# Kernel tuning notes

Hardware: AMD Instinct MI355X
Metric: run time of the kernel (lower is better)

The kernel has to match this reference:

```python
import jax, jax.numpy as jnp
import numpy as np

B = 2048       # batch
F_IN = 1024    # input feature dim
R_EMB = 1024   # rows of EmbedLinear sparse weight (new features)
NNZ_E = 65536  # nnz of embed sparse weight
F_OUT = 1024   # output dim of ExpandingLinear
NNZ_W = 131072 # nnz of main sparse weight [F_OUT, F_IN + R_EMB]
NNZ_B = 512    # nnz of sparse bias
F_MID = F_IN + R_EMB


def setup_inputs() -> dict:
    key = jax.random.key(0)
    ks = jax.random.split(key, 9)
    return {
        "x": jax.random.normal(ks[0], (B, F_IN), jnp.float32),
        "embed_rows": jax.random.randint(ks[1], (NNZ_E,), 0, R_EMB, jnp.int32),
        "embed_cols": jax.random.randint(ks[2], (NNZ_E,), 0, F_IN, jnp.int32),
        "embed_vals": jax.random.normal(ks[3], (NNZ_E,), jnp.float32) * 0.05,
        "w_rows": jax.random.randint(ks[4], (NNZ_W,), 0, F_OUT, jnp.int32),
        "w_cols": jax.random.randint(ks[5], (NNZ_W,), 0, F_MID, jnp.int32),
        "w_vals": jax.random.normal(ks[6], (NNZ_W,), jnp.float32) * 0.05,
        "bias_idx": jax.random.randint(ks[7], (NNZ_B,), 0, F_OUT, jnp.int32),
        "bias_vals": jax.random.normal(ks[8], (NNZ_B,), jnp.float32),
    }


def _spmm(rows, cols, vals, x, n_rows):
    # sparse COO [n_rows, F] @ x.T -> transposed: returns [B, n_rows]
    # (matches torch.sparse.mm(sparse_w, input.t()).t())
    g = vals[:, None] * x.T[cols]                              # [nnz, B] gather + scale
    return jax.ops.segment_sum(g, rows, num_segments=n_rows).T # scatter-add over rows


def reference(x, embed_rows, embed_cols, embed_vals,
              w_rows, w_cols, w_vals, bias_idx, bias_vals):
    # EmbedLinear.forward: sparse mm + ReLU + concat along features
    h = jax.nn.relu(_spmm(embed_rows, embed_cols, embed_vals, x, R_EMB))  # [B, R_EMB]
    x2 = jnp.concatenate([x, h], axis=1)                                   # [B, F_MID]
    # ExpandingLinear tail: sparse weight mm + densified sparse bias
    bias = jnp.zeros((F_OUT,), x.dtype).at[bias_idx].add(bias_vals)
    return _spmm(w_rows, w_cols, w_vals, x2, F_OUT) + bias[None, :]        # [B, F_OUT]
```

## Files before the change

kernel.cpp:

```cpp
#include <hip/hip_runtime.h>
#include <hip/hip_bf16.h>

#define B_SZ   2048
#define F_IN   1024
#define R_EMB  1024
#define F_OUT  1024
#define F_MID  2048
#define NNZ_E  65536
#define NNZ_W  131072
#define NNZ_B  512

typedef __bf16 bf16x8 __attribute__((ext_vector_type(8)));
typedef float  f32x4  __attribute__((ext_vector_type(4)));

__device__ inline void gload16(const void* g, void* l) {
    __builtin_amdgcn_global_load_lds(
        (const __attribute__((address_space(1))) void*)g,
        (__attribute__((address_space(3))) void*)l, 16, 0, 0);
}

__device__ inline ushort f2bf(float v) {
    __hip_bfloat16 h = __float2bfloat16(v);
    return *reinterpret_cast<ushort*>(&h);
}

__global__ void k_zero4(float4* __restrict__ p, int n) {
    int i = blockIdx.x * blockDim.x + threadIdx.x;
    if (i < n) p[i] = make_float4(0.f, 0.f, 0.f, 0.f);
}

__global__ void k_scatter_fused(const int* __restrict__ er, const int* __restrict__ ec,
                                const float* __restrict__ ev,
                                const int* __restrict__ wr_, const int* __restrict__ wc_,
                                const float* __restrict__ wv,
                                const int* __restrict__ bi, const float* __restrict__ bv,
                                float* __restrict__ Ef, float* __restrict__ Wf,
                                float* __restrict__ biasd) {
    int b = blockIdx.x, t = threadIdx.x;
    if (b < NNZ_E / 256) {
        int i = b * 256 + t;
        atomicAdd(&Ef[(size_t)er[i] * F_IN + ec[i]], ev[i]);
    } else if (b < NNZ_E / 256 + NNZ_W / 256) {
        int i = (b - NNZ_E / 256) * 256 + t;
        atomicAdd(&Wf[(size_t)wr_[i] * F_MID + wc_[i]], wv[i]);
    } else {
        int i = t;
        atomicAdd(&biasd[bi[i]], bv[i]);
        i += 256;
        atomicAdd(&biasd[bi[i]], bv[i]);
    }
}

__global__ void k_cvt_fused(const float4* __restrict__ x, ushort* __restrict__ x2,
                            const float4* __restrict__ Ef, ushort* __restrict__ Ebf,
                            const float4* __restrict__ Wf, ushort* __restrict__ Wbf) {
    int b = blockIdx.x, t = threadIdx.x;
    if (b < 2048) {
        int i = b * 256 + t;
        int row = i >> 8, c4 = i & 255;
        float4 v = x[i];
        ((ushort4*)x2)[(size_t)row * (F_MID / 4) + c4] =
            make_ushort4(f2bf(v.x), f2bf(v.y), f2bf(v.z), f2bf(v.w));
    } else if (b < 3072) {
        int i = (b - 2048) * 256 + t;
        float4 v = Ef[i];
        ((ushort4*)Ebf)[i] = make_ushort4(f2bf(v.x), f2bf(v.y), f2bf(v.z), f2bf(v.w));
    } else {
        int i = (b - 3072) * 256 + t;
        float4 v = Wf[i];
        ((ushort4*)Wbf)[i] = make_ushort4(f2bf(v.x), f2bf(v.y), f2bf(v.z), f2bf(v.w));
    }
}

template <bool RELU_BF16>
__global__ __launch_bounds__(256)
void k_gemm(const ushort* __restrict__ A, int lda,
            const ushort* __restrict__ Bm, int ldb,
            int K,
            const float* __restrict__ bias,
            float* __restrict__ outF,
            ushort* __restrict__ outH, int ldh)
{
    constexpr int BM = 64, BK = 64;
    __shared__ ushort lds[2][2][BM * BK];
    const int tid = threadIdx.x;
    const int w = tid >> 6, l = tid & 63;
    const int m0 = blockIdx.x * BM, n0 = blockIdx.y * BM;
    const int wr = w >> 1, wc = w & 1;
    const int la = l & 15;

    const int srow = w * 8 + (l >> 3);
    const int ldst = w * 512 + l * 8;

    f32x4 acc[2][2] = {};
    const int nt = K / BK;

    #define STAGE(buf, k0)                                                        \
        _Pragma("unroll")                                                         \
        for (int i = 0; i < 2; ++i) {                                             \
            int row = i * 32 + srow;                                              \
            int scol = (k0) + ((((l & 7) ^ (row & 7))) << 3);                     \
            gload16(A  + (size_t)(m0 + row) * lda + scol,                         \
                    &lds[buf][0][i * 2048 + ldst]);                               \
            gload16(Bm + (size_t)(n0 + row) * ldb + scol,                         \
                    &lds[buf][1][i * 2048 + ldst]);                               \
        }

    STAGE(0, 0);
    __syncthreads();

    for (int t = 0; t < nt; ++t) {
        const int cur = t & 1;
        if (t + 1 < nt) STAGE(cur ^ 1, (t + 1) * BK);

        const ushort* sA = &lds[cur][0][0];
        const ushort* sB = &lds[cur][1][0];
        #pragma unroll
        for (int ks = 0; ks < 2; ++ks) {
            const int k8 = ks * 4 + (l >> 4);
            bf16x8 af[2], bg[2];
            #pragma unroll
            for (int m = 0; m < 2; ++m) {
                int row = wr * 32 + m * 16 + la;
                af[m] = *(const bf16x8*)(sA + row * BK + ((k8 ^ (row & 7)) << 3));
            }
            #pragma unroll
            for (int n = 0; n < 2; ++n) {
                int row = wc * 32 + n * 16 + la;
                bg[n] = *(const bf16x8*)(sB + row * BK + ((k8 ^ (row & 7)) << 3));
            }
            #pragma unroll
            for (int m = 0; m < 2; ++m)
                #pragma unroll
                for (int n = 0; n < 2; ++n)
                    acc[m][n] = __builtin_amdgcn_mfma_f32_16x16x32_bf16(
                        af[m], bg[n], acc[m][n], 0, 0, 0);
        }
        __syncthreads();
    }

    const int lr = (l >> 4) * 4;
    #pragma unroll
    for (int m = 0; m < 2; ++m) {
        #pragma unroll
        for (int n = 0; n < 2; ++n) {
            const int col = n0 + wc * 32 + n * 16 + la;
            const float bv = RELU_BF16 ? 0.f : bias[col];
            #pragma unroll
            for (int j = 0; j < 4; ++j) {
                const int row = m0 + wr * 32 + m * 16 + lr + j;
                float v = acc[m][n][j];
                if (RELU_BF16) {
                    outH[(size_t)row * ldh + col] = f2bf(fmaxf(v, 0.f));
                } else {
                    outF[(size_t)row * F_OUT + col] = v + bv;
                }
            }
        }
    }
}

extern "C" void kernel_launch(void* const* d_in, const int* in_sizes, int n_in,
                              void* d_out, int out_size, void* d_ws, size_t ws_size,
                              hipStream_t stream) {
    const float* x          = (const float*)d_in[0];
    const int*   embed_rows = (const int*)  d_in[1];
    const int*   embed_cols = (const int*)  d_in[2];
    const float* embed_vals = (const float*)d_in[3];
    const int*   w_rows     = (const int*)  d_in[4];
    const int*   w_cols     = (const int*)  d_in[5];
    const float* w_vals     = (const float*)d_in[6];
    const int*   bias_idx   = (const int*)  d_in[7];
    const float* bias_vals  = (const float*)d_in[8];
    float* out = (float*)d_out;

    char* ws = (char*)d_ws;
    ushort* x2    = (ushort*)ws;
    float*  Wf    = (float*)(ws + (8u << 20));
    float*  Ef    = (float*)(ws + (16u << 20));
    float*  biasd = (float*)(ws + (20u << 20));
    ushort* Ebf   = (ushort*)(ws + (20u << 20) + 4096);
    ushort* Wbf   = (ushort*)(ws + (22u << 20) + 4096);

    k_zero4<<<3073, 256, 0, stream>>>((float4*)(ws + (8u << 20)), 786688);

    k_scatter_fused<<<NNZ_E / 256 + NNZ_W / 256 + 1, 256, 0, stream>>>(
        embed_rows, embed_cols, embed_vals,
        w_rows, w_cols, w_vals,
        bias_idx, bias_vals, Ef, Wf, biasd);

    k_cvt_fused<<<5120, 256, 0, stream>>>((const float4*)x, x2,
                                          (const float4*)Ef, Ebf,
                                          (const float4*)Wf, Wbf);

    k_gemm<true><<<dim3(B_SZ / 64, R_EMB / 64), 256, 0, stream>>>(
        x2, F_MID, Ebf, F_IN, F_IN, nullptr, nullptr, x2 + F_IN, F_MID);

    k_gemm<false><<<dim3(B_SZ / 64, F_OUT / 64), 256, 0, stream>>>(
        x2, F_MID, Wbf, F_MID, F_MID, biasd, out, nullptr, 0);
}
```

Before: 60.05 us.

## Enlarge GEMM tiles to 128x64x128 with 32x32 MFMA and memset zeroing

Reworks the dense GEMM to use 128x64 output tiles with a K step of 128. Each wave now computes a 64x32 sub-tile with two 32x32x16 bf16 MFMAs that share one B fragment. The goal is to cut LDS reads and global traffic per FLOP and to run fewer loop iterations. The custom zeroing kernel is replaced by hipMemsetAsync. The trade-offs are half as many blocks (256 per GEMM, which may underfill the 256 CUs), more LDS per block (96KB double-buffered), and higher register pressure from the 32 accumulator floats.

After: 71.33 us. +18.8%, slower.

```diff
diff --git a/kernel.cpp b/kernel.cpp
--- a/kernel.cpp
+++ b/kernel.cpp
@@ -11,7 +11,7 @@
 #define NNZ_B  512
 
 typedef __bf16 bf16x8 __attribute__((ext_vector_type(8)));
-typedef float  f32x4  __attribute__((ext_vector_type(4)));
+typedef float  f32x16 __attribute__((ext_vector_type(16)));
 
 __device__ inline void gload16(const void* g, void* l) {
     __builtin_amdgcn_global_load_lds(
@@ -22,11 +22,6 @@
 __device__ inline ushort f2bf(float v) {
     __hip_bfloat16 h = __float2bfloat16(v);
     return *reinterpret_cast<ushort*>(&h);
-}
-
-__global__ void k_zero4(float4* __restrict__ p, int n) {
-    int i = blockIdx.x * blockDim.x + threadIdx.x;
-    if (i < n) p[i] = make_float4(0.f, 0.f, 0.f, 0.f);
 }
 
 __global__ void k_scatter_fused(const int* __restrict__ er, const int* __restrict__ ec,
@@ -81,83 +76,81 @@
             float* __restrict__ outF,
             ushort* __restrict__ outH, int ldh)
 {
-    constexpr int BM = 64, BK = 64;
-    __shared__ ushort lds[2][2][BM * BK];
+    constexpr int BM = 128, BN = 64, BK = 128;
+    __shared__ ushort lA[2][BM * BK];
+    __shared__ ushort lB[2][BN * BK];
     const int tid = threadIdx.x;
     const int w = tid >> 6, l = tid & 63;
-    const int m0 = blockIdx.x * BM, n0 = blockIdx.y * BM;
+    const int m0 = blockIdx.x * BM, n0 = blockIdx.y * BN;
     const int wr = w >> 1, wc = w & 1;
-    const int la = l & 15;
 
-    const int srow = w * 8 + (l >> 3);
-    const int ldst = w * 512 + l * 8;
-
-    f32x4 acc[2][2] = {};
+    f32x16 acc0 = {}, acc1 = {};
     const int nt = K / BK;
 
-    #define STAGE(buf, k0)                                                        \
-        _Pragma("unroll")                                                         \
-        for (int i = 0; i < 2; ++i) {                                             \
-            int row = i * 32 + srow;                                              \
-            int scol = (k0) + ((((l & 7) ^ (row & 7))) << 3);                     \
-            gload16(A  + (size_t)(m0 + row) * lda + scol,                         \
-                    &lds[buf][0][i * 2048 + ldst]);                               \
-            gload16(Bm + (size_t)(n0 + row) * ldb + scol,                         \
-                    &lds[buf][1][i * 2048 + ldst]);                               \
+    const int srow = tid >> 4;
+    const int sslot = tid & 15;
+
+    #define STAGE(buf, k0)                                                      \
+        _Pragma("unroll")                                                       \
+        for (int i = 0; i < 8; ++i) {                                           \
+            int row = i * 16 + srow;                                            \
+            int col = (k0) + ((sslot ^ (row & 7)) << 3);                        \
+            gload16(A + (size_t)(m0 + row) * lda + col,                         \
+                    &lA[buf][i * 2048 + tid * 8]);                              \
+        }                                                                       \
+        _Pragma("unroll")                                                       \
+        for (int i = 0; i < 4; ++i) {                                           \
+            int row = i * 16 + srow;                                            \
+            int col = (k0) + ((sslot ^ (row & 7)) << 3);                        \
+            gload16(Bm + (size_t)(n0 + row) * ldb + col,                        \
+                    &lB[buf][i * 2048 + tid * 8]);                              \
         }
 
     STAGE(0, 0);
     __syncthreads();
 
+    const int ra0 = wr * 64 + (l & 31);
+    const int ra1 = ra0 + 32;
+    const int rb  = wc * 32 + (l & 31);
+    const int xa  = (ra0 & 7), xb = (rb & 7);
+
     for (int t = 0; t < nt; ++t) {
         const int cur = t & 1;
         if (t + 1 < nt) STAGE(cur ^ 1, (t + 1) * BK);
 
-        const ushort* sA = &lds[cur][0][0];
-        const ushort* sB = &lds[cur][1][0];
+        const ushort* sA = &lA[cur][0];
+        const ushort* sB = &lB[cur][0];
         #pragma unroll
-        for (int ks = 0; ks < 2; ++ks) {
-            const int k8 = ks * 4 + (l >> 4);
-            bf16x8 af[2], bg[2];
-            #pragma unroll
-            for (int m = 0; m < 2; ++m) {
-                int row = wr * 32 + m * 16 + la;
-                af[m] = *(const bf16x8*)(sA + row * BK + ((k8 ^ (row & 7)) << 3));
-            }
-            #pragma unroll
-            for (int n = 0; n < 2; ++n) {
-                int row = wc * 32 + n * 16 + la;
-                bg[n] = *(const bf16x8*)(sB + row * BK + ((k8 ^ (row & 7)) << 3));
-            }
-            #pragma unroll
-            for (int m = 0; m < 2; ++m)
-                #pragma unroll
-                for (int n = 0; n < 2; ++n)
-                    acc[m][n] = __builtin_amdgcn_mfma_f32_16x16x32_bf16(
-                        af[m], bg[n], acc[m][n], 0, 0, 0);
+        for (int ks = 0; ks < 8; ++ks) {
+            const int c = ks * 2 + (l >> 5);
+            bf16x8 af0 = *(const bf16x8*)(sA + ra0 * BK + ((c ^ xa) << 3));
+            bf16x8 af1 = *(const bf16x8*)(sA + ra1 * BK + ((c ^ xa) << 3));
+            bf16x8 bg  = *(const bf16x8*)(sB + rb  * BK + ((c ^ xb) << 3));
+            acc0 = __builtin_amdgcn_mfma_f32_32x32x16_bf16(af0, bg, acc0, 0, 0, 0);
+            acc1 = __builtin_amdgcn_mfma_f32_32x32x16_bf16(af1, bg, acc1, 0, 0, 0);
         }
         __syncthreads();
     }
 
-    const int lr = (l >> 4) * 4;
-    #pragma unroll
-    for (int m = 0; m < 2; ++m) {
+    const int col = n0 + wc * 32 + (l & 31);
+    const int r0  = m0 + wr * 64 + 4 * (l >> 5);
+    if (RELU_BF16) {
         #pragma unroll
-        for (int n = 0; n < 2; ++n) {
-            const int col = n0 + wc * 32 + n * 16 + la;
-            const float bv = RELU_BF16 ? 0.f : bias[col];
-            #pragma unroll
-            for (int j = 0; j < 4; ++j) {
-                const int row = m0 + wr * 32 + m * 16 + lr + j;
-                float v = acc[m][n][j];
-                if (RELU_BF16) {
-                    outH[(size_t)row * ldh + col] = f2bf(fmaxf(v, 0.f));
-                } else {
-                    outF[(size_t)row * F_OUT + col] = v + bv;
-                }
-            }
+        for (int r = 0; r < 16; ++r) {
+            int row = r0 + (r & 3) + 8 * (r >> 2);
+            outH[(size_t)row * ldh + col]        = f2bf(fmaxf(acc0[r], 0.f));
+            outH[(size_t)(row + 32) * ldh + col] = f2bf(fmaxf(acc1[r], 0.f));
+        }
+    } else {
+        const float bv = bias[col];
+        #pragma unroll
+        for (int r = 0; r < 16; ++r) {
+            int row = r0 + (r & 3) + 8 * (r >> 2);
+            outF[(size_t)row * F_OUT + col]        = acc0[r] + bv;
+            outF[(size_t)(row + 32) * F_OUT + col] = acc1[r] + bv;
         }
     }
+    #undef STAGE
 }
 
 extern "C" void kernel_launch(void* const* d_in, const int* in_sizes, int n_in,
@@ -182,7 +175,7 @@
     ushort* Ebf   = (ushort*)(ws + (20u << 20) + 4096);
     ushort* Wbf   = (ushort*)(ws + (22u << 20) + 4096);
 
-    k_zero4<<<3073, 256, 0, stream>>>((float4*)(ws + (8u << 20)), 786688);
+    hipMemsetAsync(ws + (8u << 20), 0, (12u << 20) + 4096, stream);
 
     k_scatter_fused<<<NNZ_E / 256 + NNZ_W / 256 + 1, 256, 0, stream>>>(
         embed_rows, embed_cols, embed_vals,
@@ -193,9 +186,9 @@
                                           (const float4*)Ef, Ebf,
                                           (const float4*)Wf, Wbf);
 
-    k_gemm<true><<<dim3(B_SZ / 64, R_EMB / 64), 256, 0, stream>>>(
+    k_gemm<true><<<dim3(B_SZ / 128, R_EMB / 64), 256, 0, stream>>>(
         x2, F_MID, Ebf, F_IN, F_IN, nullptr, nullptr, x2 + F_IN, F_MID);
 
-    k_gemm<false><<<dim3(B_SZ / 64, F_OUT / 64), 256, 0, stream>>>(
+    k_gemm<false><<<dim3(B_SZ / 128, F_OUT / 64), 256, 0, stream>>>(
         x2, F_MID, Wbf, F_MID, F_MID, biasd, out, nullptr, 0);
 }
```

## Split output GEMM K-range so x-part runs concurrently with embed GEMM

Applied to the files above, without the earlier changes.

Splits the second GEMM along K: the half that multiplies the original x columns runs in the same launch as the embed GEMM, and only the half depending on the ReLU output runs afterward, accumulating into out. The aim is a wider first grid, so the GPU is fuller and the dependent second GEMM is shorter. The cost is a read-modify-write of the fp32 output in the second phase and branchy mode selection inside the kernel.

Result: faster. 55.36 us (-7.8%).

```diff
diff --git a/kernel.cpp b/kernel.cpp
--- a/kernel.cpp
+++ b/kernel.cpp
@@ -72,35 +72,47 @@
     }
 }
 
-template <bool RELU_BF16>
+template <int PHASE>
 __global__ __launch_bounds__(256)
-void k_gemm(const ushort* __restrict__ A, int lda,
-            const ushort* __restrict__ Bm, int ldb,
-            int K,
-            const float* __restrict__ bias,
-            float* __restrict__ outF,
-            ushort* __restrict__ outH, int ldh)
+void k_gemm3(const ushort* __restrict__ x2,
+             const ushort* __restrict__ Ebf,
+             const ushort* __restrict__ Wbf,
+             const float* __restrict__ biasd,
+             float* __restrict__ out,
+             ushort* __restrict__ hOut)
 {
-    constexpr int BM = 64, BK = 64;
-    __shared__ ushort lds[2][2][BM * BK];
+    constexpr int BS = 64, BK = 64, NT = 1024 / BK;
+    __shared__ ushort lds[2][2][BS * BK];
     const int tid = threadIdx.x;
     const int w = tid >> 6, l = tid & 63;
-    const int m0 = blockIdx.x * BM, n0 = blockIdx.y * BM;
     const int wr = w >> 1, wc = w & 1;
     const int la = l & 15;
+    const int m0 = blockIdx.x * BS;
+
+    int mode, ldb, n0;
+    const ushort* A;
+    const ushort* Bm;
+    if (PHASE == 0) {
+        if (blockIdx.y < 16) {
+            mode = 0; A = x2;        Bm = Ebf;        ldb = F_IN;  n0 = blockIdx.y * BS;
+        } else {
+            mode = 1; A = x2;        Bm = Wbf;        ldb = F_MID; n0 = (blockIdx.y - 16) * BS;
+        }
+    } else {
+        mode = 2;     A = x2 + F_IN; Bm = Wbf + F_IN; ldb = F_MID; n0 = blockIdx.y * BS;
+    }
 
     const int srow = w * 8 + (l >> 3);
     const int ldst = w * 512 + l * 8;
 
     f32x4 acc[2][2] = {};
-    const int nt = K / BK;
 
     #define STAGE(buf, k0)                                                        \
         _Pragma("unroll")                                                         \
         for (int i = 0; i < 2; ++i) {                                             \
             int row = i * 32 + srow;                                              \
             int scol = (k0) + ((((l & 7) ^ (row & 7))) << 3);                     \
-            gload16(A  + (size_t)(m0 + row) * lda + scol,                         \
+            gload16(A  + (size_t)(m0 + row) * F_MID + scol,                       \
                     &lds[buf][0][i * 2048 + ldst]);                               \
             gload16(Bm + (size_t)(n0 + row) * ldb + scol,                         \
                     &lds[buf][1][i * 2048 + ldst]);                               \
@@ -109,9 +121,9 @@
     STAGE(0, 0);
     __syncthreads();
 
-    for (int t = 0; t < nt; ++t) {
+    for (int t = 0; t < NT; ++t) {
         const int cur = t & 1;
-        if (t + 1 < nt) STAGE(cur ^ 1, (t + 1) * BK);
+        if (t + 1 < NT) STAGE(cur ^ 1, (t + 1) * BK);
 
         const ushort* sA = &lds[cur][0][0];
         const ushort* sB = &lds[cur][1][0];
@@ -138,6 +150,7 @@
         }
         __syncthreads();
     }
+    #undef STAGE
 
     const int lr = (l >> 4) * 4;
     #pragma unroll
@@ -145,15 +158,24 @@
         #pragma unroll
         for (int n = 0; n < 2; ++n) {
             const int col = n0 + wc * 32 + n * 16 + la;
-            const float bv = RELU_BF16 ? 0.f : bias[col];
-            #pragma unroll
-            for (int j = 0; j < 4; ++j) {
-                const int row = m0 + wr * 32 + m * 16 + lr + j;
-                float v = acc[m][n][j];
-                if (RELU_BF16) {
-                    outH[(size_t)row * ldh + col] = f2bf(fmaxf(v, 0.f));
-                } else {
-                    outF[(size_t)row * F_OUT + col] = v + bv;
+            if (mode == 0) {
+                #pragma unroll
+                for (int j = 0; j < 4; ++j) {
+                    int row = m0 + wr * 32 + m * 16 + lr + j;
+                    hOut[(size_t)row * F_MID + col] = f2bf(fmaxf(acc[m][n][j], 0.f));
+                }
+            } else if (mode == 1) {
+                const float bv = biasd[col];
+                #pragma unroll
+                for (int j = 0; j < 4; ++j) {
+                    int row = m0 + wr * 32 + m * 16 + lr + j;
+                    out[(size_t)row * F_OUT + col] = acc[m][n][j] + bv;
+                }
+            } else {
+                #pragma unroll
+                for (int j = 0; j < 4; ++j) {
+                    int row = m0 + wr * 32 + m * 16 + lr + j;
+                    out[(size_t)row * F_OUT + col] += acc[m][n][j];
                 }
             }
         }
@@ -193,9 +215,9 @@
                                           (const float4*)Ef, Ebf,
                                           (const float4*)Wf, Wbf);
 
-    k_gemm<true><<<dim3(B_SZ / 64, R_EMB / 64), 256, 0, stream>>>(
-        x2, F_MID, Ebf, F_IN, F_IN, nullptr, nullptr, x2 + F_IN, F_MID);
-
-    k_gemm<false><<<dim3(B_SZ / 64, F_OUT / 64), 256, 0, stream>>>(
-        x2, F_MID, Wbf, F_MID, F_MID, biasd, out, nullptr, 0);
-}
+    k_gemm3<0><<<dim3(B_SZ / 64, 32), 256, 0, stream>>>(
+        x2, Ebf, Wbf, biasd, out, x2 + F_IN);
+
+    k_gemm3<1><<<dim3(B_SZ / 64, 16), 256, 0, stream>>>(
+        x2, Ebf, Wbf, biasd, out, x2 + F_IN);
+}
```
